# Kernel optimization log

Measured on AMD Instinct MI355X. Metric: run time of the kernel, lower is better.

## Reference

```python
import jax, jax.numpy as jnp
import numpy as np

N = 1024
V = 3889   # SMAL mesh vertices
NJ = 33    # kinematic-tree joints
NR = 35    # rotations in theta (35*3 = 105)
NB = 41    # shape betas
PARENTS = np.concatenate([[0], np.arange(NJ - 1)]).astype(np.int32)  # parent[i] < i
EXTRA_VERT_IDS = np.array([1863, 26, 2124, 150, 3055, 1097])


def _beta_scale_mask():
    m = np.zeros((NR, 3, 6), np.float32)
    leg = list(range(7, 15)) + list(range(17, 25))
    tail = list(range(25, 32))
    ears = [33, 34]
    m[leg, 2, 0] = 1.0; m[leg, 0, 1] = 1.0; m[leg, 1, 1] = 1.0
    m[tail, 0, 2] = 1.0; m[tail, 1, 3] = 1.0; m[tail, 2, 3] = 1.0
    m[ears, 1, 4] = 1.0; m[ears, 2, 5] = 1.0
    return jnp.asarray(m.reshape(NR * 3, 6).T)  # (6, 105)

BETA_SCALE_MASK = _beta_scale_mask()


def batch_rodrigues(theta):
    # theta: (M, 3) axis-angle -> (M, 3, 3) rotation matrices
    angle = jnp.linalg.norm(theta + 1e-8, axis=1, keepdims=True)  # (M,1)
    r = theta / angle
    c = jnp.cos(angle)[..., None]
    s = jnp.sin(angle)[..., None]
    outer = r[:, :, None] * r[:, None, :]
    z = jnp.zeros_like(r[:, 0])
    rx, ry, rz = r[:, 0], r[:, 1], r[:, 2]
    H = jnp.stack([z, -rz, ry, rz, z, -rx, -ry, rx, z], axis=1).reshape(-1, 3, 3)
    eye = jnp.eye(3, dtype=theta.dtype)
    return c * eye + (1.0 - c) * outer + s * H


def make_A(R, t):
    # R: (n,3,3), t: (n,3) -> homogeneous (n,4,4)
    top = jnp.concatenate([R, t[..., None]], axis=-1)
    bottom = jnp.broadcast_to(jnp.array([0.0, 0.0, 0.0, 1.0], dtype=R.dtype), (R.shape[0], 1, 4))
    return jnp.concatenate([top, bottom], axis=1)


def smal_forward(beta, theta, trans, betas_logscale, shapedirs, v_template, J_regressor, posedirs, weights):
    n = beta.shape[0]
    v_shaped = v_template + (beta @ shapedirs).reshape(n, V, 3)           # (n,V,3)
    J = jnp.einsum('nva,vj->nja', v_shaped, J_regressor)                  # (n,33,3)
    Rs = batch_rodrigues(theta.reshape(-1, 3)).reshape(n, NR, 3, 3)
    # pose blendshape term: original multiplies an all-zero pose_feature by posedirs
    v_posed = v_shaped + (jnp.zeros((1, 288), v_shaped.dtype) @ posedirs).reshape(1, V, 3)
    # per-joint anisotropic log-scales
    scal = jnp.exp(betas_logscale @ BETA_SCALE_MASK).reshape(n, NR, 3)    # (n,35,3)
    # kinematic chain (fixed 33-joint loop with parent dependency)
    results = [make_A(Rs[:, 0], J[:, 0])]
    for i in range(1, NJ):
        p = int(PARENTS[i])
        j_here = J[:, i] - J[:, p]
        # diag(1/s_parent) @ R @ diag(s_i), exact inverse of diagonal scale
        rot_new = Rs[:, i] * scal[:, i][:, None, :] / scal[:, p][:, :, None]
        results.append(results[p] @ make_A(rot_new, j_here))
    results = jnp.stack(results, axis=1)                                   # (n,33,4,4)
    init_bone = jnp.einsum('njxk,njk->njx', results[..., :3], J)           # (n,33,4)
    A = jnp.concatenate([results[..., :3], (results[..., 3] - init_bone)[..., None]], axis=-1)
    # linear blend skinning
    T = jnp.einsum('vj,njk->nvk', weights, A.reshape(n, NJ, 16)).reshape(n, V, 4, 4)
    v_homo = jnp.concatenate([v_posed * jnp.ones((n, 1, 1), v_posed.dtype),
                              jnp.ones((n, V, 1), v_posed.dtype)], axis=-1)
    verts = jnp.einsum('nvab,nvb->nva', T, v_homo)[..., :3] + trans[:, None, :]
    joints = jnp.einsum('nva,vj->nja', verts, J_regressor)                 # (n,33,3)
    joints = jnp.concatenate([joints, verts[:, EXTRA_VERT_IDS]], axis=1)   # (n,39,3)
    return verts, joints


def setup_inputs() -> dict:
    key = jax.random.key(0)
    ks = jax.random.split(key, 9)
    return {
        'beta': jax.random.normal(ks[0], (N, NB), jnp.float32) * 0.1,
        'theta': jax.random.normal(ks[1], (N, NR * 3), jnp.float32) * 0.2,
        'trans': jax.random.normal(ks[2], (N, 3), jnp.float32),
        'betas_logscale': jax.random.normal(ks[3], (N, 6), jnp.float32) * 0.1,
        'shapedirs': jax.random.normal(ks[4], (NB, V * 3), jnp.float32) * 0.01,
        'v_template': jax.random.normal(ks[5], (V, 3), jnp.float32),
        'J_regressor': jax.random.uniform(ks[6], (V, NJ), jnp.float32) / V,
        'posedirs': jax.random.normal(ks[7], (288, V * 3), jnp.float32) * 0.01,
        'weights': jax.random.uniform(ks[8], (V, NJ), jnp.float32),
    }


def reference(beta, theta, trans, betas_logscale, shapedirs, v_template, J_regressor, posedirs, weights):
    return smal_forward(beta, theta, trans, betas_logscale, shapedirs, v_template, J_regressor, posedirs, weights)
```

## Files before the change

kernel.cpp:

```cpp
#include <hip/hip_runtime.h>
#include <hip/hip_bf16.h>

#define NV 3889
#define NV3 11667
#define NVP 3904
#define NVAP 11712
#define NJC 33
#define NBB 41
#define NN 1024

__device__ const int EXTRA_IDS[6] = {1863, 26, 2124, 150, 3055, 1097};

#define WS_SJ    0
#define WS_WPK   4160
#define WS_SDPK  129088
#define WS_BPK   503872
#define WS_APK   536640
#define WS_JTL   929856
#define WS_VTL   1028160
#define WS_SJP   13611072

typedef __attribute__((ext_vector_type(8))) short short8v;
typedef __attribute__((ext_vector_type(4))) float f32x4;

__device__ __forceinline__ ushort bf16bits(float x) {
  __hip_bfloat16 h = __float2bfloat16(x);
  return *reinterpret_cast<ushort*>(&h);
}

#define PREP_SJ_BLOCKS 672
#define PREP_SD_BLOCKS 366
#define PREP_PK_BLOCKS 250
#define PREP_VZ_BLOCKS 576
__global__ void __launch_bounds__(256) k_prep(
    const float* __restrict__ Jreg, const float* __restrict__ w,
    const float* __restrict__ beta, const float* __restrict__ sd,
    const float* __restrict__ vt, float* __restrict__ ws) {
  int bx = blockIdx.x;
  int t = threadIdx.x;
  if (bx < PREP_SJ_BLOCKS) {
    int bid2 = bx;
    int b = bid2 >> 4, c = bid2 & 15;
    const float* src = (b < NBB) ? (sd + (size_t)b * NV3) : vt;
    int dv = t / 33, j = t - dv * 33;
    float p0 = 0.f, p1 = 0.f, p2 = 0.f;
    int vbase = c * 244;
    int vend = vbase + 244;
    if (vend > NV) vend = NV;
    if (t < 231) {
      for (int v0 = vbase; v0 < vend; v0 += 7) {
        int v = v0 + dv;
        if (v < vend) {
          float jr = Jreg[v0 * 33 + t];
          p0 += src[v * 3 + 0] * jr;
          p1 += src[v * 3 + 1] * jr;
          p2 += src[v * 3 + 2] * jr;
        }
      }
    }
    __shared__ float sred[7][33][3];
    if (t < 231) { sred[dv][j][0] = p0; sred[dv][j][1] = p1; sred[dv][j][2] = p2; }
    __syncthreads();
    if (t < 99) {
      int jj = t / 3, aa = t - jj * 3;
      float s = 0.f;
#pragma unroll
      for (int d = 0; d < 7; d++) s += sred[d][jj][aa];
      ws[WS_SJP + bid2 * 100 + t] = s;
    }
    return;
  }
  bx -= PREP_SJ_BLOCKS;
  if (bx < PREP_SD_BLOCKS) {
    __shared__ ushort tl[32 * 50];
    int va0 = bx * 32;
    for (int i = t; i < 42 * 32; i += 256) {
      int bs = i >> 5, off = i & 31;
      int va = va0 + off;
      float v = 0.f;
      if (va < NV3) v = (bs < NBB) ? sd[(size_t)bs * NV3 + va] : vt[va];
      tl[off * 50 + bs] = bf16bits(v);
    }
    __syncthreads();
    int va_l = t >> 3, ch = t & 7;
    short8v pk;
#pragma unroll
    for (int e = 0; e < 8; e++) {
      int bs = ch * 8 + e;
      pk[e] = (bs < 42) ? (short)tl[va_l * 50 + bs] : (short)0;
    }
    *(short8v*)((ushort*)(ws + WS_SDPK) + ((size_t)(va0 + va_l) * 64 + ch * 8)) = pk;
    return;
  }
  bx -= PREP_SD_BLOCKS;
  if (bx < PREP_PK_BLOCKS) {
    int id8 = bx * 256 + t;
    const int R1 = NVP * 64 / 8;
    const int R3 = NN * 64 / 8;
    short8v pk;
    if (id8 < R1) {
      int u = id8 * 8;
      int v = u >> 6, j0 = u & 63;
#pragma unroll
      for (int e = 0; e < 8; e++) {
        int j = j0 + e;
        float val;
        if (j < NJC)      val = (v < NV) ? w[v * NJC + j] : 0.f;
        else if (j == 41) val = 1.f;
        else              val = 0.f;
        pk[e] = (short)bf16bits(val);
      }
      *(short8v*)((ushort*)(ws + WS_WPK) + u) = pk;
      return;
    }
    id8 -= R1;
    if (id8 < R3) {
      int u = id8 * 8;
      int n = u >> 6, bs0 = u & 63;
#pragma unroll
      for (int e = 0; e < 8; e++) {
        int bs = bs0 + e;
        float val = (bs < NBB) ? beta[n * NBB + bs] : (bs == NBB ? 1.f : 0.f);
        pk[e] = (short)bf16bits(val);
      }
      *(short8v*)((ushort*)(ws + WS_BPK) + u) = pk;
      return;
    }
    id8 -= R3;
    {
      int u = id8 * 8;
      int tile = u >> 9, lane = (u >> 3) & 63;
      int jt = tile >> 7, kc = tile & 127;
      int j = jt * 16 + (lane & 15);
      int vb = kc * 32 + ((lane >> 4) << 3);
#pragma unroll
      for (int e = 0; e < 8; e++) {
        int v = vb + e;
        float val = (j < NJC && v < NV) ? Jreg[v * NJC + j] : 0.f;
        pk[e] = (short)bf16bits(val);
      }
      *(short8v*)((ushort*)(ws + WS_JTL) + u) = pk;
      return;
    }
  }
  bx -= PREP_PK_BLOCKS;
  {
    int id8 = bx * 256 + t;
    int plane = id8 / 768;
    int rem8 = id8 - plane * 768;
    short8v z = {0, 0, 0, 0, 0, 0, 0, 0};
    *(short8v*)((ushort*)(ws + WS_VTL) +
                ((size_t)plane * 131072 + 124928 + rem8 * 8)) = z;
  }
}

__global__ void __launch_bounds__(256) k_sjr(float* __restrict__ ws) {
  int idx = blockIdx.x * 256 + threadIdx.x;
  if (idx >= 42 * 99) return;
  int b = idx / 99, k = idx - b * 99;
  float s = 0.f;
#pragma unroll
  for (int c = 0; c < 16; c++) s += ws[WS_SJP + (b * 16 + c) * 100 + k];
  ws[WS_SJ + idx] = s;
}

__device__ __forceinline__ void get_scal(int r, float e0, float e1, float e2, float e3,
                                         float s[3]) {
  bool leg  = (r >= 7 && r <= 14) || (r >= 17 && r <= 24);
  bool tail = (r >= 25 && r <= 31);
  s[0] = leg ? e1 : (tail ? e2 : 1.f);
  s[1] = leg ? e1 : (tail ? e3 : 1.f);
  s[2] = leg ? e0 : (tail ? e3 : 1.f);
}

__device__ __forceinline__ void rodrigues(const float* th, float R[9]) {
  float tx = th[0], ty = th[1], tz = th[2];
  float ax = tx + 1e-8f, ay = ty + 1e-8f, az = tz + 1e-8f;
  float angle = sqrtf(ax * ax + ay * ay + az * az);
  float inv = 1.f / angle;
  float rx = tx * inv, ry = ty * inv, rz = tz * inv;
  float c = cosf(angle), s = sinf(angle), o = 1.f - c;
  R[0] = c + o * rx * rx;      R[1] = o * rx * ry - s * rz; R[2] = o * rx * rz + s * ry;
  R[3] = o * rx * ry + s * rz; R[4] = c + o * ry * ry;      R[5] = o * ry * rz - s * rx;
  R[6] = o * rx * rz - s * ry; R[7] = o * ry * rz + s * rx; R[8] = c + o * rz * rz;
}

__global__ void __launch_bounds__(128) k_pose(
    const float* __restrict__ beta, const float* __restrict__ theta,
    const float* __restrict__ bls, const float* __restrict__ trans,
    float* __restrict__ ws) {
  int n = blockIdx.x, t = threadIdx.x;
  __shared__ float Jsh[99];
  __shared__ float Bsh[NJC * 12];
  __shared__ float Ash[NJC * 12];
  if (t < 99) {
    const float* SJ = ws + WS_SJ;
    float acc = SJ[NBB * 99 + t];
    const float* bn = beta + n * NBB;
#pragma unroll
    for (int b = 0; b < NBB; b++) acc += bn[b] * SJ[b * 99 + t];
    Jsh[t] = acc;
  }
  __syncthreads();
  if (t < NJC) {
    float R[9];
    rodrigues(theta + n * 105 + t * 3, R);
    float* B = Bsh + t * 12;
    if (t == 0) {
      B[0] = R[0]; B[1] = R[1]; B[2]  = R[2]; B[3]  = Jsh[0];
      B[4] = R[3]; B[5] = R[4]; B[6]  = R[5]; B[7]  = Jsh[1];
      B[8] = R[6]; B[9] = R[7]; B[10] = R[8]; B[11] = Jsh[2];
    } else {
      float e0 = expf(bls[n * 6 + 0]), e1 = expf(bls[n * 6 + 1]);
      float e2 = expf(bls[n * 6 + 2]), e3 = expf(bls[n * 6 + 3]);
      float si[3], sp[3];
      get_scal(t, e0, e1, e2, e3, si);
      get_scal(t - 1, e0, e1, e2, e3, sp);
#pragma unroll
      for (int r = 0; r < 3; r++) {
        float inv = 1.f / sp[r];
#pragma unroll
        for (int cc = 0; cc < 3; cc++) B[r * 4 + cc] = R[r * 3 + cc] * si[cc] * inv;
        B[r * 4 + 3] = Jsh[t * 3 + r] - Jsh[(t - 1) * 3 + r];
      }
    }
  }
  __syncthreads();
  if (t == 0) {
    float G[12];
#pragma unroll
    for (int k = 0; k < 12; k++) G[k] = Bsh[k];
#pragma unroll
    for (int i = 0; i < NJC; i++) {
      if (i > 0) {
        float b[12];
#pragma unroll
        for (int k = 0; k < 12; k++) b[k] = Bsh[i * 12 + k];
        float Gn[12];
#pragma unroll
        for (int r = 0; r < 3; r++) {
#pragma unroll
          for (int cc = 0; cc < 4; cc++) {
            float acc = G[r * 4 + 0] * b[0 * 4 + cc] + G[r * 4 + 1] * b[1 * 4 + cc] +
                        G[r * 4 + 2] * b[2 * 4 + cc];
            if (cc == 3) acc += G[r * 4 + 3];
            Gn[r * 4 + cc] = acc;
          }
        }
#pragma unroll
        for (int k = 0; k < 12; k++) G[k] = Gn[k];
      }
      float jx = Jsh[i * 3 + 0], jy = Jsh[i * 3 + 1], jz = Jsh[i * 3 + 2];
      float* Ai = Ash + i * 12;
      Ai[0] = G[0]; Ai[1] = G[1]; Ai[2]  = G[2];
      Ai[3] = G[3] - (G[0] * jx + G[1] * jy + G[2] * jz);
      Ai[4] = G[4]; Ai[5] = G[5]; Ai[6]  = G[6];
      Ai[7] = G[7] - (G[4] * jx + G[5] * jy + G[6] * jz);
      Ai[8] = G[8]; Ai[9] = G[9]; Ai[10] = G[10];
      Ai[11] = G[11] - (G[8] * jx + G[9] * jy + G[10] * jz);
    }
  }
  __syncthreads();
  __hip_bfloat16* apk = (__hip_bfloat16*)(ws + WS_APK) + (size_t)n * 768;
  for (int i = t; i < 768; i += 128) {
    int c = i >> 6, j = i & 63;
    float val = 0.f;
    if (j < NJC)                           val = Ash[j * 12 + c];
    else if (j == 41 && (c & 3) == 3)      val = trans[n * 3 + (c >> 2)];
    apk[i] = __float2bfloat16(val);
  }
}

#define ASH_USH (16 * 12 * 72)
#define VSL2_USH (2 * 16 * 72)

__global__ void __launch_bounds__(512, 4) k_sv(
    const float* __restrict__ ws, ushort* __restrict__ vst,
    float* __restrict__ out) {
  __shared__ __align__(16) ushort lds[ASH_USH + 8 * VSL2_USH];
  int wv = threadIdx.x >> 6, lane = threadIdx.x & 63;
  int g = lane >> 4, c16 = lane & 15;
  int p = blockIdx.x * 8 + wv;
  int pc = p < 122 ? p : 121;
  bool pok = p < 122;
  int vtA = pc * 2, vtB = vtA + 1;
  int vA = vtA * 16 + c16, vB = vtB * 16 + c16;
  int nb0 = blockIdx.y * 32;
  const ushort* Wp = (const ushort*)(ws + WS_WPK);
  const ushort* Sp = (const ushort*)(ws + WS_SDPK);
  const ushort* Bp = (const ushort*)(ws + WS_BPK);
  const ushort* Ap = (const ushort*)(ws + WS_APK);

  short8v wfA0 = *(const short8v*)(Wp + vA * 64 + g * 8);
  short8v wfA1 = *(const short8v*)(Wp + vA * 64 + 32 + g * 8);
  short8v wfB0 = *(const short8v*)(Wp + vB * 64 + g * 8);
  short8v wfB1 = *(const short8v*)(Wp + vB * 64 + 32 + g * 8);
  int vaA = vtA * 48 + c16, vaB = vtB * 48 + c16;

  ushort* vslA = lds + ASH_USH + wv * VSL2_USH;
  ushort* vslB = vslA + 1152;
  bool act = g < 3;
  int hiA = c16 >> 3, hiB = 2 + (c16 >> 3), e8 = c16 & 7;

#pragma unroll 1
  for (int ch = 0; ch < 2; ch++) {
    int nb = nb0 + ch * 16;
    {
      const uint4* srcq = (const uint4*)(Ap + (size_t)nb * 768);
      for (int e = threadIdx.x; e < 1536; e += 512) {
        int r = e >> 3, col = e & 7;
        uint4 x = srcq[e];
        *(uint4*)(lds + r * 72 + col * 8) = x;
      }
    }
    short8v bf0 = *(const short8v*)(Bp + (size_t)(nb + c16) * 64 + g * 8);
    short8v bf1 = *(const short8v*)(Bp + (size_t)(nb + c16) * 64 + 32 + g * 8);
    short8v sfA00 = *(const short8v*)(Sp + (size_t)(vaA +  0) * 64 + g * 8);
    short8v sfA01 = *(const short8v*)(Sp + (size_t)(vaA +  0) * 64 + 32 + g * 8);
    short8v sfA10 = *(const short8v*)(Sp + (size_t)(vaA + 16) * 64 + g * 8);
    short8v sfA11 = *(const short8v*)(Sp + (size_t)(vaA + 16) * 64 + 32 + g * 8);
    short8v sfA20 = *(const short8v*)(Sp + (size_t)(vaA + 32) * 64 + g * 8);
    short8v sfA21 = *(const short8v*)(Sp + (size_t)(vaA + 32) * 64 + 32 + g * 8);
    short8v sfB00 = *(const short8v*)(Sp + (size_t)(vaB +  0) * 64 + g * 8);
    short8v sfB01 = *(const short8v*)(Sp + (size_t)(vaB +  0) * 64 + 32 + g * 8);
    short8v sfB10 = *(const short8v*)(Sp + (size_t)(vaB + 16) * 64 + g * 8);
    short8v sfB11 = *(const short8v*)(Sp + (size_t)(vaB + 16) * 64 + 32 + g * 8);
    short8v sfB20 = *(const short8v*)(Sp + (size_t)(vaB + 32) * 64 + g * 8);
    short8v sfB21 = *(const short8v*)(Sp + (size_t)(vaB + 32) * 64 + 32 + g * 8);
    f32x4 aA0 = {0,0,0,0}, aA1 = {0,0,0,0}, aA2 = {0,0,0,0};
    f32x4 aB0 = {0,0,0,0}, aB1 = {0,0,0,0}, aB2 = {0,0,0,0};
    aA0 = __builtin_amdgcn_mfma_f32_16x16x32_bf16(sfA00, bf0, aA0, 0, 0, 0);
    aA0 = __builtin_amdgcn_mfma_f32_16x16x32_bf16(sfA01, bf1, aA0, 0, 0, 0);
    aA1 = __builtin_amdgcn_mfma_f32_16x16x32_bf16(sfA10, bf0, aA1, 0, 0, 0);
    aA1 = __builtin_amdgcn_mfma_f32_16x16x32_bf16(sfA11, bf1, aA1, 0, 0, 0);
    aA2 = __builtin_amdgcn_mfma_f32_16x16x32_bf16(sfA20, bf0, aA2, 0, 0, 0);
    aA2 = __builtin_amdgcn_mfma_f32_16x16x32_bf16(sfA21, bf1, aA2, 0, 0, 0);
    aB0 = __builtin_amdgcn_mfma_f32_16x16x32_bf16(sfB00, bf0, aB0, 0, 0, 0);
    aB0 = __builtin_amdgcn_mfma_f32_16x16x32_bf16(sfB01, bf1, aB0, 0, 0, 0);
    aB1 = __builtin_amdgcn_mfma_f32_16x16x32_bf16(sfB10, bf0, aB1, 0, 0, 0);
    aB1 = __builtin_amdgcn_mfma_f32_16x16x32_bf16(sfB11, bf1, aB1, 0, 0, 0);
    aB2 = __builtin_amdgcn_mfma_f32_16x16x32_bf16(sfB20, bf0, aB2, 0, 0, 0);
    aB2 = __builtin_amdgcn_mfma_f32_16x16x32_bf16(sfB21, bf1, aB2, 0, 0, 0);
    {
      int wb = c16 * 72;
#pragma unroll
      for (int r = 0; r < 4; r++) {
        int rho = g * 4 + r;
        vslA[wb + (rho / 3) * 4 + (rho % 3)] = bf16bits(aA0[r]);
        vslB[wb + (rho / 3) * 4 + (rho % 3)] = bf16bits(aB0[r]);
      }
#pragma unroll
      for (int r = 0; r < 4; r++) {
        int rho = 16 + g * 4 + r;
        vslA[wb + (rho / 3) * 4 + (rho % 3)] = bf16bits(aA1[r]);
        vslB[wb + (rho / 3) * 4 + (rho % 3)] = bf16bits(aB1[r]);
      }
#pragma unroll
      for (int r = 0; r < 4; r++) {
        int rho = 32 + g * 4 + r;
        vslA[wb + (rho / 3) * 4 + (rho % 3)] = bf16bits(aA2[r]);
        vslB[wb + (rho / 3) * 4 + (rho % 3)] = bf16bits(aB2[r]);
      }
    }
    __syncthreads();

    int nt_w = nb >> 4;
    size_t tbg = ((size_t)((act ? g : 0) * 64 + nt_w) * 128 + pc) * 1024;
#pragma unroll 4
    for (int np = 0; np < 16; np++) {
      const ushort* an = lds + np * 864 + c16 * 72 + g * 8;
      short8v af0 = *(const short8v*)(an);
      short8v af1 = *(const short8v*)(an + 32);
      f32x4 accA = {0,0,0,0}, accB = {0,0,0,0};
      accA = __builtin_amdgcn_mfma_f32_16x16x32_bf16(af0, wfA0, accA, 0, 0, 0);
      accA = __builtin_amdgcn_mfma_f32_16x16x32_bf16(af1, wfA1, accA, 0, 0, 0);
      accB = __builtin_amdgcn_mfma_f32_16x16x32_bf16(af0, wfB0, accB, 0, 0, 0);
      accB = __builtin_amdgcn_mfma_f32_16x16x32_bf16(af1, wfB1, accB, 0, 0, 0);
      uint2 qA = *(const uint2*)(vslA + np * 72 + c16 * 4);
      uint2 qB = *(const uint2*)(vslB + np * 72 + c16 * 4);
      float sxA = __uint_as_float((qA.x & 0xffffu) << 16);
      float syA = __uint_as_float(qA.x & 0xffff0000u);
      float szA = __uint_as_float((qA.y & 0xffffu) << 16);
      float sxB = __uint_as_float((qB.x & 0xffffu) << 16);
      float syB = __uint_as_float(qB.x & 0xffff0000u);
      float szB = __uint_as_float((qB.y & 0xffffu) << 16);
      float rA = fmaf(accA[0], sxA, fmaf(accA[1], syA, fmaf(accA[2], szA, accA[3])));
      float rB = fmaf(accB[0], sxB, fmaf(accB[1], syB, fmaf(accB[2], szB, accB[3])));
      if (pok && act) {
        vst[tbg + (size_t)((hiA * 16 + np) * 8 + e8)] = bf16bits(rA);
        vst[tbg + (size_t)((hiB * 16 + np) * 8 + e8)] = bf16bits(rB);
        out[((size_t)(nb + np) * NV + vA) * 3 + g] = rA;
        if (vB < NV) out[((size_t)(nb + np) * NV + vB) * 3 + g] = rB;
      }
    }
    __syncthreads();
  }
}

__global__ void __launch_bounds__(512) k_jg2(
    const float* __restrict__ ws, const float* __restrict__ verts,
    float* __restrict__ jout) {
  __shared__ float red[8][48][16];
  int nt = blockIdx.x, a = blockIdx.y;
  int wv = threadIdx.x >> 6, lane = threadIdx.x & 63;
  const ushort* Jt = (const ushort*)(ws + WS_JTL);
  const ushort* Vt = (const ushort*)(ws + WS_VTL) + ((size_t)(a * 64 + nt) << 17);
  f32x4 acc0 = {0,0,0,0};
  f32x4 acc1 = {0,0,0,0};
  f32x4 acc2 = {0,0,0,0};
#pragma unroll 4
  for (int i = 0; i < 16; i++) {
    int kc = wv * 16 + i;
    short8v bfr = *(const short8v*)(Vt + ((size_t)kc << 10) + lane * 8);
    short8v af0 = *(const short8v*)(Jt + ((size_t)(0 * 128 + kc) << 9) + lane * 8);
    short8v af1 = *(const short8v*)(Jt + ((size_t)(1 * 128 + kc) << 9) + lane * 8);
    short8v af2 = *(const short8v*)(Jt + ((size_t)(2 * 128 + kc) << 9) + lane * 8);
    acc0 = __builtin_amdgcn_mfma_f32_16x16x32_bf16(af0, bfr, acc0, 0, 0, 0);
    acc1 = __builtin_amdgcn_mfma_f32_16x16x32_bf16(af1, bfr, acc1, 0, 0, 0);
    acc2 = __builtin_amdgcn_mfma_f32_16x16x32_bf16(af2, bfr, acc2, 0, 0, 0);
  }
  int hi = lane >> 4, c16 = lane & 15;
#pragma unroll
  for (int r = 0; r < 4; r++) {
    red[wv][ 0 + hi * 4 + r][c16] = acc0[r];
    red[wv][16 + hi * 4 + r][c16] = acc1[r];
    red[wv][32 + hi * 4 + r][c16] = acc2[r];
  }
  __syncthreads();
  for (int idx = threadIdx.x; idx < NJC * 16; idx += 512) {
    int j = idx >> 4, np = idx & 15;
    float s = red[0][j][np] + red[1][j][np] + red[2][j][np] + red[3][j][np] +
              red[4][j][np] + red[5][j][np] + red[6][j][np] + red[7][j][np];
    jout[(nt * 16 + np) * 117 + j * 3 + a] = s;
  }
  if (threadIdx.x < 96) {
    int e = threadIdx.x >> 4, np = threadIdx.x & 15;
    int n = nt * 16 + np;
    jout[n * 117 + 99 + e * 3 + a] = verts[(size_t)n * NV3 + EXTRA_IDS[e] * 3 + a];
  }
}

extern "C" void kernel_launch(void* const* d_in, const int* in_sizes, int n_in,
                              void* d_out, int out_size, void* d_ws, size_t ws_size,
                              hipStream_t stream) {
  const float* beta       = (const float*)d_in[0];
  const float* theta      = (const float*)d_in[1];
  const float* trans      = (const float*)d_in[2];
  const float* bls        = (const float*)d_in[3];
  const float* shapedirs  = (const float*)d_in[4];
  const float* v_template = (const float*)d_in[5];
  const float* Jreg       = (const float*)d_in[6];
  const float* weights    = (const float*)d_in[8];
  float* out = (float*)d_out;
  float* ws  = (float*)d_ws;
  float* jout = out + (size_t)NN * NV3;

  k_prep<<<PREP_SJ_BLOCKS + PREP_SD_BLOCKS + PREP_PK_BLOCKS + PREP_VZ_BLOCKS,
           256, 0, stream>>>(Jreg, weights, beta, shapedirs, v_template, ws);
  k_sjr<<<17, 256, 0, stream>>>(ws);
  k_pose<<<NN, 128, 0, stream>>>(beta, theta, bls, trans, ws);
  dim3 gsv(16, 32);
  k_sv<<<gsv, 512, 0, stream>>>(ws, (ushort*)(ws + WS_VTL), out);
  dim3 gj(64, 3);
  k_jg2<<<gj, 512, 0, stream>>>(ws, out, jout);
}
```

Baseline: 70.29 us.

## Fuse SJ reduction into pose kernel and batch 16 samples per block

Removes the separate k_sjr launch by having each k_pose block redundantly reduce the 42x99 shape-joint partials into shared memory. Each block now processes 16 samples with 256 threads, running 16 kinematic chains in parallel lanes instead of one per block, and writes the bf16 A-packing as 8-wide vector stores. This trades a kernel launch and serial per-sample chain for redundant reduction work (64 blocks each reading the partials) and only 64 blocks of occupancy.

```diff
diff --git a/kernel.cpp b/kernel.cpp
--- a/kernel.cpp
+++ b/kernel.cpp
@@ -154,16 +154,6 @@
   }
 }
 
-__global__ void __launch_bounds__(256) k_sjr(float* __restrict__ ws) {
-  int idx = blockIdx.x * 256 + threadIdx.x;
-  if (idx >= 42 * 99) return;
-  int b = idx / 99, k = idx - b * 99;
-  float s = 0.f;
-#pragma unroll
-  for (int c = 0; c < 16; c++) s += ws[WS_SJP + (b * 16 + c) * 100 + k];
-  ws[WS_SJ + idx] = s;
-}
-
 __device__ __forceinline__ void get_scal(int r, float e0, float e1, float e2, float e3,
                                          float s[3]) {
   bool leg  = (r >= 7 && r <= 14) || (r >= 17 && r <= 24);
@@ -185,57 +175,70 @@
   R[6] = o * rx * rz - s * ry; R[7] = o * ry * rz + s * rx; R[8] = c + o * rz * rz;
 }
 
-__global__ void __launch_bounds__(128) k_pose(
+__global__ void __launch_bounds__(256) k_pose(
     const float* __restrict__ beta, const float* __restrict__ theta,
     const float* __restrict__ bls, const float* __restrict__ trans,
     float* __restrict__ ws) {
-  int n = blockIdx.x, t = threadIdx.x;
-  __shared__ float Jsh[99];
-  __shared__ float Bsh[NJC * 12];
-  __shared__ float Ash[NJC * 12];
-  if (t < 99) {
-    const float* SJ = ws + WS_SJ;
-    float acc = SJ[NBB * 99 + t];
+  int nb = blockIdx.x * 16;
+  int t = threadIdx.x;
+  __shared__ float SJsh[42 * 99];
+  __shared__ float Jsh[16][99];
+  __shared__ float Bsh[16][NJC * 12];
+  for (int idx = t; idx < 42 * 99; idx += 256) {
+    int b = idx / 99, k = idx - b * 99;
+    float s = 0.f;
+#pragma unroll
+    for (int c = 0; c < 16; c++) s += ws[WS_SJP + (b * 16 + c) * 100 + k];
+    SJsh[idx] = s;
+  }
+  __syncthreads();
+  for (int idx = t; idx < 16 * 99; idx += 256) {
+    int row = idx / 99, k = idx - row * 99;
+    int n = nb + row;
+    float acc = SJsh[NBB * 99 + k];
     const float* bn = beta + n * NBB;
 #pragma unroll
-    for (int b = 0; b < NBB; b++) acc += bn[b] * SJ[b * 99 + t];
-    Jsh[t] = acc;
+    for (int b = 0; b < NBB; b++) acc += bn[b] * SJsh[b * 99 + k];
+    Jsh[row][k] = acc;
   }
   __syncthreads();
-  if (t < NJC) {
+  for (int idx = t; idx < 16 * NJC; idx += 256) {
+    int row = idx / NJC, i = idx - row * NJC;
+    int n = nb + row;
     float R[9];
-    rodrigues(theta + n * 105 + t * 3, R);
-    float* B = Bsh + t * 12;
-    if (t == 0) {
-      B[0] = R[0]; B[1] = R[1]; B[2]  = R[2]; B[3]  = Jsh[0];
-      B[4] = R[3]; B[5] = R[4]; B[6]  = R[5]; B[7]  = Jsh[1];
-      B[8] = R[6]; B[9] = R[7]; B[10] = R[8]; B[11] = Jsh[2];
+    rodrigues(theta + n * 105 + i * 3, R);
+    float* B = Bsh[row] + i * 12;
+    if (i == 0) {
+      B[0] = R[0]; B[1] = R[1]; B[2]  = R[2]; B[3]  = Jsh[row][0];
+      B[4] = R[3]; B[5] = R[4]; B[6]  = R[5]; B[7]  = Jsh[row][1];
+      B[8] = R[6]; B[9] = R[7]; B[10] = R[8]; B[11] = Jsh[row][2];
     } else {
       float e0 = expf(bls[n * 6 + 0]), e1 = expf(bls[n * 6 + 1]);
       float e2 = expf(bls[n * 6 + 2]), e3 = expf(bls[n * 6 + 3]);
       float si[3], sp[3];
-      get_scal(t, e0, e1, e2, e3, si);
-      get_scal(t - 1, e0, e1, e2, e3, sp);
+      get_scal(i, e0, e1, e2, e3, si);
+      get_scal(i - 1, e0, e1, e2, e3, sp);
 #pragma unroll
       for (int r = 0; r < 3; r++) {
         float inv = 1.f / sp[r];
 #pragma unroll
         for (int cc = 0; cc < 3; cc++) B[r * 4 + cc] = R[r * 3 + cc] * si[cc] * inv;
-        B[r * 4 + 3] = Jsh[t * 3 + r] - Jsh[(t - 1) * 3 + r];
+        B[r * 4 + 3] = Jsh[row][i * 3 + r] - Jsh[row][(i - 1) * 3 + r];
       }
     }
   }
   __syncthreads();
-  if (t == 0) {
+  if (t < 16) {
+    int row = t;
     float G[12];
 #pragma unroll
-    for (int k = 0; k < 12; k++) G[k] = Bsh[k];
+    for (int k = 0; k < 12; k++) G[k] = Bsh[row][k];
 #pragma unroll
     for (int i = 0; i < NJC; i++) {
       if (i > 0) {
         float b[12];
 #pragma unroll
-        for (int k = 0; k < 12; k++) b[k] = Bsh[i * 12 + k];
+        for (int k = 0; k < 12; k++) b[k] = Bsh[row][i * 12 + k];
         float Gn[12];
 #pragma unroll
         for (int r = 0; r < 3; r++) {
@@ -250,8 +253,8 @@
 #pragma unroll
         for (int k = 0; k < 12; k++) G[k] = Gn[k];
       }
-      float jx = Jsh[i * 3 + 0], jy = Jsh[i * 3 + 1], jz = Jsh[i * 3 + 2];
-      float* Ai = Ash + i * 12;
+      float jx = Jsh[row][i * 3 + 0], jy = Jsh[row][i * 3 + 1], jz = Jsh[row][i * 3 + 2];
+      float* Ai = Bsh[row] + i * 12;
       Ai[0] = G[0]; Ai[1] = G[1]; Ai[2]  = G[2];
       Ai[3] = G[3] - (G[0] * jx + G[1] * jy + G[2] * jz);
       Ai[4] = G[4]; Ai[5] = G[5]; Ai[6]  = G[6];
@@ -261,13 +264,20 @@
     }
   }
   __syncthreads();
-  __hip_bfloat16* apk = (__hip_bfloat16*)(ws + WS_APK) + (size_t)n * 768;
-  for (int i = t; i < 768; i += 128) {
-    int c = i >> 6, j = i & 63;
-    float val = 0.f;
-    if (j < NJC)                           val = Ash[j * 12 + c];
-    else if (j == 41 && (c & 3) == 3)      val = trans[n * 3 + (c >> 2)];
-    apk[i] = __float2bfloat16(val);
+  for (int idx = t; idx < 16 * 96; idx += 256) {
+    int row = idx / 96, r2 = idx - row * 96;
+    int c = r2 >> 3, jg = r2 & 7;
+    int n = nb + row;
+    short8v pk;
+#pragma unroll
+    for (int e = 0; e < 8; e++) {
+      int j = jg * 8 + e;
+      float val = 0.f;
+      if (j < NJC)                      val = Bsh[row][j * 12 + c];
+      else if (j == 41 && (c & 3) == 3) val = trans[n * 3 + (c >> 2)];
+      pk[e] = (short)bf16bits(val);
+    }
+    *(short8v*)((ushort*)(ws + WS_APK) + (size_t)n * 768 + c * 64 + jg * 8) = pk;
   }
 }
 
@@ -457,8 +467,7 @@
 
   k_prep<<<PREP_SJ_BLOCKS + PREP_SD_BLOCKS + PREP_PK_BLOCKS + PREP_VZ_BLOCKS,
            256, 0, stream>>>(Jreg, weights, beta, shapedirs, v_template, ws);
-  k_sjr<<<17, 256, 0, stream>>>(ws);
-  k_pose<<<NN, 128, 0, stream>>>(beta, theta, bls, trans, ws);
+  k_pose<<<64, 256, 0, stream>>>(beta, theta, bls, trans, ws);
   dim3 gsv(16, 32);
   k_sv<<<gsv, 512, 0, stream>>>(ws, (ushort*)(ws + WS_VTL), out);
   dim3 gj(64, 3);
```

Result: slower. 76.86 us (+9.3%).
